# Optimization experiments

Measured on AMD Instinct MI355X. Metric: run time of the kernel, lower is better.

## Reference

```python
import math
import jax, jax.numpy as jnp
from jax import lax
import numpy as np

C = 256; A = 3; NIMG = 2; L = 5
SIZES = [(200, 304), (100, 152), (50, 76), (25, 38), (13, 19)]
STRIDES = [4, 8, 16, 32, 64]
LVTOP = 600          # cfg['lvtop'] (eval)
IMTOP = 300          # cfg['imtop1'] (eval)
SCORE_THR = 0.0      # cfg['score_thr1']
MIN_SIZE = 1e-2      # cfg['min_size1']
IOU_THR = 0.7        # cfg['iou_thr1']
IMH, IMW = 800.0, 1216.0
BBOX_CLIP = math.log(1000.0 / 16.0)   # clamp=True in decode_boxes
GROUP_OFF = 4096.0                     # > max canvas coord -> disjoint NMS groups


def _level_anchors(h, w, stride):
    scale = stride * 8.0
    r = np.array([0.5, 1.0, 2.0])
    ws = scale * np.sqrt(r); hs = scale / np.sqrt(r)          # [A]
    ys, xs = np.meshgrid(np.arange(h), np.arange(w), indexing='ij')
    cx = (xs.reshape(-1, 1) + 0.5) * stride                    # [HW,1]
    cy = (ys.reshape(-1, 1) + 0.5) * stride
    a = np.stack([cx - ws / 2, cy - hs / 2, cx + ws / 2, cy + hs / 2], axis=-1)
    return a.reshape(-1, 4).astype(np.float32)                 # [HW*A,4]


def setup_inputs() -> dict:
    key = jax.random.key(0)
    ks = jax.random.split(key, 10)
    inp = {}
    for i, (h, w) in enumerate(SIZES):
        inp[f'fmap{i}'] = jax.random.normal(ks[i], (NIMG, C, h, w), jnp.float32)
        inp[f'priors{i}'] = jnp.asarray(_level_anchors(h, w, STRIDES[i]))
    inp['imsizes'] = jnp.array([[IMH, IMW]] * NIMG, jnp.float32)   # (h, w) per image
    inp['conv_w'] = jax.random.normal(ks[5], (C, C, 3, 3), jnp.float32) * 0.03
    inp['conv_b'] = jnp.zeros((C,), jnp.float32)
    inp['log_w'] = jax.random.normal(ks[6], (A, C), jnp.float32) * 0.03
    inp['log_b'] = jnp.zeros((A,), jnp.float32)
    inp['reg_w'] = jax.random.normal(ks[7], (A * 4, C), jnp.float32) * 0.01
    inp['reg_b'] = jnp.zeros((A * 4,), jnp.float32)
    return inp


def _decode(reg, pri):
    pw = pri[..., 2] - pri[..., 0]; ph = pri[..., 3] - pri[..., 1]
    pcx = pri[..., 0] + 0.5 * pw;   pcy = pri[..., 1] + 0.5 * ph
    dx, dy = reg[..., 0], reg[..., 1]
    dw = jnp.minimum(reg[..., 2], BBOX_CLIP)
    dh = jnp.minimum(reg[..., 3], BBOX_CLIP)
    cx = dx * pw + pcx; cy = dy * ph + pcy
    w = pw * jnp.exp(dw); h = ph * jnp.exp(dh)
    return jnp.stack([cx - 0.5 * w, cy - 0.5 * h, cx + 0.5 * w, cy + 0.5 * h], axis=-1)


def _forward(fmaps, priors, imsizes, conv_w, conv_b, log_w, log_b, reg_w, reg_b):
    dn = ('NCHW', 'OIHW', 'NCHW')
    boxes_l, score_l = [], []
    for x, pri in zip(fmaps, priors):
        n = x.shape[0]
        h = jax.nn.relu(lax.conv_general_dilated(x, conv_w, (1, 1), 'SAME',
                                                 dimension_numbers=dn)
                        + conv_b[None, :, None, None])
        logit = (jnp.einsum('nchw,ac->nahw', h, log_w)
                 + log_b[None, :, None, None]).transpose(0, 2, 3, 1).reshape(n, -1)
        reg = (jnp.einsum('nchw,ac->nahw', h, reg_w)
               + reg_b[None, :, None, None]).transpose(0, 2, 3, 1).reshape(n, -1, 4)
        vals, top = lax.top_k(logit, LVTOP)                        # per-level topk
        reg_g = jnp.take_along_axis(reg, jnp.broadcast_to(top[:, :, None], (n, LVTOP, 4)), axis=1)
        pri_g = pri[top]                                           # [n,k,4]
        boxes_l.append(_decode(reg_g, pri_g))
        score_l.append(jax.nn.sigmoid(vals))
    boxes = jnp.concatenate(boxes_l, axis=1)                       # [n, L*k, 4]
    obj = jnp.concatenate(score_l, axis=1)                         # [n, L*k]
    n, dim = boxes.shape[0], boxes.shape[1]
    Nall = n * dim
    boxes = boxes.reshape(Nall, 4); obj = obj.reshape(Nall)
    imidx = jnp.arange(Nall) // dim
    lvl = jnp.tile(jnp.repeat(jnp.arange(L), LVTOP), n)
    valid = obj >= SCORE_THR
    sz = imsizes[imidx]                                            # [Nall,2] (h,w)
    boxes = jnp.stack([jnp.clip(boxes[:, 0], 0.0, sz[:, 1]),
                       jnp.clip(boxes[:, 1], 0.0, sz[:, 0]),
                       jnp.clip(boxes[:, 2], 0.0, sz[:, 1]),
                       jnp.clip(boxes[:, 3], 0.0, sz[:, 0])], axis=-1)
    valid = valid & (boxes[:, 2] - boxes[:, 0] >= MIN_SIZE) & (boxes[:, 3] - boxes[:, 1] >= MIN_SIZE)
    groups = imidx * 10 + lvl                                      # batched_nms groups
    # sort by score, invalid entries pushed to the end
    order = jnp.argsort(-jnp.where(valid, obj, -1.0))
    b = boxes[order]; v = valid[order]; g = groups[order]; im = imidx[order]
    # group-offset trick == torchvision batched_nms
    ob = b + g.astype(b.dtype)[:, None] * GROUP_OFF
    area = (ob[:, 2] - ob[:, 0]) * (ob[:, 3] - ob[:, 1])
    lt = jnp.maximum(ob[:, None, :2], ob[None, :, :2])
    rb = jnp.minimum(ob[:, None, 2:], ob[None, :, 2:])
    wh = jnp.maximum(rb - lt, 0.0)
    inter = wh[..., 0] * wh[..., 1]
    iou = lax.stop_gradient(inter / (area[:, None] + area[None, :] - inter))
    idxr = jnp.arange(Nall)
    def body(i, keep):
        sup = jnp.any(keep & (iou[i] > IOU_THR) & (idxr < i))
        return keep.at[i].set(v[i] & ~sup)
    keep = lax.fori_loop(0, Nall, body, jnp.zeros((Nall,), bool))
    # per-image cap at IMTOP (keep is already in score order)
    sel = keep[None, :] & (im[None, :] == jnp.arange(n)[:, None])  # [n,Nall]
    sel = sel & (jnp.cumsum(sel, axis=1) <= IMTOP)
    prio = jnp.where(sel, Nall - idxr[None, :], 0)
    pvals, pos = lax.top_k(prio, IMTOP)                            # [n,IMTOP]
    vout = pvals > 0
    bout = jnp.where(vout[..., None], b[pos], 0.0)                 # [n,IMTOP,4]
    imout = jnp.broadcast_to(jnp.arange(n)[:, None], (n, IMTOP)).reshape(-1).astype(jnp.int32)
    return bout.reshape(-1, 4), imout, vout.reshape(-1)


def reference(fmap0, fmap1, fmap2, fmap3, fmap4,
              priors0, priors1, priors2, priors3, priors4,
              imsizes, conv_w, conv_b, log_w, log_b, reg_w, reg_b):
    return _forward([fmap0, fmap1, fmap2, fmap3, fmap4],
                    [priors0, priors1, priors2, priors3, priors4],
                    imsizes, conv_w, conv_b, log_w, log_b, reg_w, reg_b)
```

## Files before the change

kernel.cpp:

```cpp
#include <hip/hip_runtime.h>
#include <math.h>

typedef unsigned long long u64;
typedef unsigned int u32;
typedef unsigned short u16;
typedef _Float16 f16;
typedef __attribute__((ext_vector_type(8))) _Float16 f16x8;
typedef __attribute__((ext_vector_type(8))) unsigned short ushort8;
typedef __attribute__((ext_vector_type(4))) float f32x4;

#define LVTOP 600
#define IMTOP 300
#define NIMG 2
#define NLVL 5
#define NCAND (NLVL*LVTOP)

__constant__ int d_HW[5]    = {60800,15200,3800,950,247};
__constant__ int d_LGOFF[5] = {0,364800,456000,478800,484500};
__constant__ int d_RGOFF[5] = {0,1459200,1824000,1915200,1938000};
__constant__ int d_H[5]  = {200,100,50,25,13};
__constant__ int d_W[5]  = {304,152,76,38,19};
__constant__ int d_TX[5] = {5,3,2,1,1};
__constant__ long d_XB[5] = {0, 31129600, 38912000, 40857600, 41344000};
__constant__ long d_CB[5] = {0, 3891200, 4864000, 5107200, 5168000};
__constant__ int d_SB[6] = {0,64,80,84,85,86};
#define NCHUNK 5183808
#define WS_NEED 178889200ull

__device__ __forceinline__ u32 okey(float f){
  u32 u = __float_as_uint(f);
  return (u & 0x80000000u) ? ~u : (u | 0x80000000u);
}

__device__ __forceinline__ void f16_split(float v, u16& hb, u16& lb){
  f16 h = (f16)v;
  float r = v - (float)h;
  f16 l = (f16)r;
  hb = __builtin_bit_cast(u16, h);
  lb = __builtin_bit_cast(u16, l);
}

__device__ __forceinline__ u64 shfl64(u64 v, int src){
  u32 lo = __shfl((u32)v, src);
  u32 hi = __shfl((u32)(v >> 32), src);
  return ((u64)hi << 32) | lo;
}

__device__ __forceinline__ void dma16(const u16* g, u16* l){
  __builtin_amdgcn_global_load_lds(
      (const __attribute__((address_space(1))) u32*)g,
      (__attribute__((address_space(3))) u32*)l, 16, 0, 0);
}

template<int NN, int NT>
__device__ void bitonic_desc64(u64* a, int tid){
  for (int k = 2; k <= NN; k <<= 1){
    for (int j = k >> 1; j > 0; j >>= 1){
      __syncthreads();
      for (int i = tid; i < NN; i += NT){
        int ixj = i ^ j;
        if (ixj > i){
          u64 x = a[i], y = a[ixj];
          bool up = ((i & k) == 0);
          if (up ? (x < y) : (x > y)){ a[i] = y; a[ixj] = x; }
        }
      }
    }
  }
  __syncthreads();
}

template<int NN, int NT>
__device__ void bitonic_asc32(u32* a, int tid){
  for (int k = 2; k <= NN; k <<= 1){
    for (int j = k >> 1; j > 0; j >>= 1){
      __syncthreads();
      for (int i = tid; i < NN; i += NT){
        int ixj = i ^ j;
        if (ixj > i){
          u32 x = a[i], y = a[ixj];
          bool up = ((i & k) == 0);
          if (up ? (x > y) : (x < y)){ a[i] = y; a[ixj] = x; }
        }
      }
    }
  }
  __syncthreads();
}

__device__ void suffix_scan(u32* s, int NB, int tid){
  for (int off = 1; off < NB; off <<= 1){
    u32 v0 = 0, v1 = 0;
    int i1 = tid + 1024;
    if (tid < NB) v0 = s[tid] + ((tid + off < NB) ? s[tid + off] : 0u);
    if (i1  < NB) v1 = s[i1]  + ((i1  + off < NB) ? s[i1  + off] : 0u);
    __syncthreads();
    if (tid < NB) s[tid] = v0;
    if (i1  < NB) s[i1]  = v1;
    __syncthreads();
  }
}

__global__ __launch_bounds__(256) void wprep(
    const float* __restrict__ cw, const float* __restrict__ lw,
    const float* __restrict__ rw, u16* __restrict__ wT, u16* __restrict__ whB,
    u32* __restrict__ ghist)
{
  int t = threadIdx.x;
  if (blockIdx.x < 72){
    int id = blockIdx.x*256 + t;
    int cc = id & 7;
    int co = (id >> 3) & 255;
    int tap = id >> 11;
    int ntg = co >> 4;
    size_t base = (size_t)((tap*8 + cc)*16 + ntg) * 1024;
    #pragma unroll
    for (int ci = 0; ci < 32; ci++){
      float v = cw[(size_t)co*2304 + (size_t)(cc*32 + ci)*9 + tap];
      u16 hi, lo; f16_split(v, hi, lo);
      int q = ci >> 3, j = ci & 7;
      int lane = q*16 + (co & 15);
      wT[base + lane*8 + j] = hi;
      wT[base + 512 + lane*8 + j] = lo;
    }
  } else if (blockIdx.x == 72){
    if (t < 128){
      int ks = t >> 4, nn = t & 15;
      for (int ci = 0; ci < 32; ci++){
        int k = ks*32 + ci;
        float v = 0.0f;
        if (nn < 3) v = lw[nn*256 + k];
        else if (nn < 15) v = rw[(nn-3)*256 + k];
        u16 hi, lo; f16_split(v, hi, lo);
        int q = ci >> 3, j = ci & 7;
        int lane = q*16 + nn;
        whB[ks*1024 + lane*8 + j] = hi;
        whB[ks*1024 + 512 + lane*8 + j] = lo;
      }
    }
  } else {
    int z = (blockIdx.x - 73)*1024 + t;
    #pragma unroll
    for (int q = 0; q < 4; q++){
      int i = z + q*256;
      if (i < NLVL*NIMG*2048) ghist[i] = 0;
    }
  }
}

__global__ __launch_bounds__(256) void xsplit(
    const float* __restrict__ f0, const float* __restrict__ f1,
    const float* __restrict__ f2, const float* __restrict__ f3,
    const float* __restrict__ f4,
    u16* __restrict__ xh, u16* __restrict__ xl, u16* __restrict__ zp)
{
  long id = (long)blockIdx.x*256 + threadIdx.x;
  if (blockIdx.x == 0 && threadIdx.x < 8) zp[threadIdx.x] = 0;
  if (id >= NCHUNK) return;
  int l = (id < d_CB[1]) ? 0 : (id < d_CB[2]) ? 1 : (id < d_CB[3]) ? 2 : (id < d_CB[4]) ? 3 : 4;
  long rem = id - d_CB[l];
  int HW = d_HW[l];
  int n = (int)(rem / (32*HW));
  int r2 = (int)(rem - (long)n*32*HW);
  int cg = r2 / HW;
  int p = r2 - cg*HW;
  const float* fm = (l==0)?f0:(l==1)?f1:(l==2)?f2:(l==3)?f3:f4;
  const float* gp = fm + ((size_t)(n*256 + cg*8))*HW + p;
  ushort8 hv, lv;
  #pragma unroll
  for (int j = 0; j < 8; j++){
    float v = gp[(size_t)j*HW];
    u16 hb, lb; f16_split(v, hb, lb);
    hv[j] = hb; lv[j] = lb;
  }
  *(ushort8*)&xh[id*8] = hv;
  *(ushort8*)&xl[id*8] = lv;
}

__global__ __launch_bounds__(256, 3) void conv_mfma(
    const float* __restrict__ f0, const float* __restrict__ f1,
    const float* __restrict__ f2, const float* __restrict__ f3,
    const float* __restrict__ f4,
    const u16* __restrict__ xh, const u16* __restrict__ xl,
    const u16* __restrict__ zp,
    const u16* __restrict__ wT, const u16* __restrict__ whB,
    const float* __restrict__ cb, const float* __restrict__ lb,
    const float* __restrict__ rb,
    float* __restrict__ lgb, float* __restrict__ rgb, int use_dma)
{
  __shared__ __align__(16) u16 smem[26624];

  const int t = threadIdx.x;
  const int n = blockIdx.y;
  int bx = blockIdx.x;
  int l, rbk;
  if (bx < 1000){ l = 0; rbk = bx; }
  else if (bx < 1300){ l = 1; rbk = bx - 1000; }
  else if (bx < 1400){ l = 2; rbk = bx - 1300; }
  else if (bx < 1425){ l = 3; rbk = bx - 1400; }
  else { l = 4; rbk = bx - 1425; }
  const int H = d_H[l], W = d_W[l], tilesX = d_TX[l];
  const int ty = rbk / tilesX;
  const int x0 = (rbk - ty*tilesX) * 64;
  const float* fm = (l==0) ? f0 : (l==1) ? f1 : (l==2) ? f2 : (l==3) ? f3 : f4;

  const int wave = t >> 6, lane = t & 63;
  const int quad = lane >> 4, l15 = lane & 15;
  const int HWp = H * W;
  const float* xin = fm + (size_t)n * 256 * HWp;

  f32x4 acc[4][4];
  #pragma unroll
  for (int a = 0; a < 4; a++)
    #pragma unroll
    for (int b = 0; b < 4; b++) acc[a][b] = (f32x4){0.f,0.f,0.f,0.f};

  auto compute_cc = [&](int cc, int bufo){
    #pragma unroll
    for (int ky = 0; ky < 3; ky++){
      #pragma unroll
      for (int kx = 0; kx < 3; kx++){
        int o0 = bufo + ((quad*3 + ky)*68 + (l15 + kx))*8;
        f16x8 Ah[4], Al[4];
        #pragma unroll
        for (int mt = 0; mt < 4; mt++){
          Ah[mt] = *(const f16x8*)&smem[o0 + mt*128];
          Al[mt] = *(const f16x8*)&smem[o0 + 6656 + mt*128];
        }
        const u16* bt = wT + (size_t)((((ky*3+kx)*8 + cc)*16) + wave*4) * 1024 + lane*8;
        #pragma unroll
        for (int nt = 0; nt < 4; nt++){
          f16x8 Bh = *(const f16x8*)(bt + nt*1024);
          f16x8 Bl = *(const f16x8*)(bt + nt*1024 + 512);
          #pragma unroll
          for (int mt = 0; mt < 4; mt++){
            acc[mt][nt] = __builtin_amdgcn_mfma_f32_16x16x32_f16(Ah[mt], Bh, acc[mt][nt], 0,0,0);
            acc[mt][nt] = __builtin_amdgcn_mfma_f32_16x16x32_f16(Al[mt], Bh, acc[mt][nt], 0,0,0);
            acc[mt][nt] = __builtin_amdgcn_mfma_f32_16x16x32_f16(Ah[mt], Bl, acc[mt][nt], 0,0,0);
          }
        }
      }
    }
  };

  if (use_dma){
    const u16* ph[4]; const u16* pl[4]; u32 pstep[4]; int dsth[4]; int kv[4];
    #pragma unroll
    for (int s = 0; s < 4; s++){
      int k = wave + s*4;
      kv[s] = (k < 13);
      int g = k*64 + lane;
      int gg = (g < 816) ? g : 0;
      int cg = gg / 204; int rem = gg - cg*204;
      int r = rem / 68;  int xi = rem - r*68;
      int gy = ty - 1 + r, gx = x0 - 1 + xi;
      bool inb = (g < 816) && (gy >= 0) && (gy < H) && (gx >= 0) && (gx < W);
      int gy2 = gy < 0 ? 0 : (gy >= H ? H-1 : gy);
      int gx2 = gx < 0 ? 0 : (gx >= W ? W-1 : gx);
      long off = d_XB[l] + (((long)(n*32 + cg))*HWp + (long)gy2*W + gx2)*8;
      ph[s] = inb ? (xh + off) : zp;
      pl[s] = inb ? (xl + off) : zp;
      pstep[s] = inb ? (u32)(32*HWp) : 0u;
      dsth[s] = k*512;
    }
    auto stage = [&](int bufo){
      #pragma unroll
      for (int s = 0; s < 4; s++){
        if (kv[s]){
          dma16(ph[s], &smem[bufo + dsth[s]]);
          dma16(pl[s], &smem[bufo + 6656 + dsth[s]]);
          ph[s] += pstep[s]; pl[s] += pstep[s];
        }
      }
    };
    stage(0);
    __syncthreads();
    for (int cc = 0; cc < 8; cc++){
      if (cc < 7) stage(((cc+1)&1)*13312);
      compute_cc(cc, (cc&1)*13312);
      __syncthreads();
    }
  } else {
    for (int cc = 0; cc < 8; cc++){
      __syncthreads();
      #pragma unroll
      for (int it = 0; it < 4; it++){
        int G = t + it*256;
        if (G < 816){
          int cg = G / 204; int rem = G - cg*204;
          int r = rem / 68; int xi = rem - r*68;
          int gy = ty - 1 + r, gx = x0 - 1 + xi;
          bool inb = (gy >= 0) & (gy < H) & (gx >= 0) & (gx < W);
          const float* gp = xin + (size_t)(cc*32 + cg*8) * HWp
                          + (size_t)(gy < 0 ? 0 : gy) * W + (gx < 0 ? 0 : gx);
          ushort8 hv, lv;
          #pragma unroll
          for (int j = 0; j < 8; j++){
            float v = inb ? gp[(size_t)j * HWp] : 0.0f;
            u16 hb, lb2; f16_split(v, hb, lb2);
            hv[j] = hb; lv[j] = lb2;
          }
          int off = ((cg*3 + r)*68 + xi)*8;
          *(ushort8*)&smem[off] = hv;
          *(ushort8*)&smem[6656 + off] = lv;
        }
      }
      __syncthreads();
      compute_cc(cc, 0);
    }
    __syncthreads();
  }

  u16* hA_h = smem;
  u16* hA_l = smem + 8704;
  f32x4 a2 = (f32x4){0.f,0.f,0.f,0.f};
  #pragma unroll
  for (int half = 0; half < 2; half++){
    if ((wave >> 1) == half){
      #pragma unroll
      for (int mt = 0; mt < 4; mt++){
        #pragma unroll
        for (int nt = 0; nt < 4; nt++){
          int col = (wave & 1)*64 + nt*16 + l15;
          float bias = cb[half*128 + col];
          #pragma unroll
          for (int r = 0; r < 4; r++){
            float h = fmaxf(acc[mt][nt][r] + bias, 0.0f);
            u16 hb, lb2; f16_split(h, hb, lb2);
            int pos = mt*16 + quad*4 + r;
            hA_h[pos*136 + col] = hb;
            hA_l[pos*136 + col] = lb2;
          }
        }
      }
    }
    __syncthreads();
    #pragma unroll
    for (int ks2 = 0; ks2 < 4; ks2++){
      int ks = half*4 + ks2;
      int ao = (wave*16 + l15)*136 + ks2*32 + quad*8;
      f16x8 Ah = *(const f16x8*)&hA_h[ao];
      f16x8 Al = *(const f16x8*)&hA_l[ao];
      const u16* wb = whB + ks*1024 + lane*8;
      f16x8 Bh = *(const f16x8*)wb;
      f16x8 Bl = *(const f16x8*)(wb + 512);
      a2 = __builtin_amdgcn_mfma_f32_16x16x32_f16(Ah, Bh, a2, 0,0,0);
      a2 = __builtin_amdgcn_mfma_f32_16x16x32_f16(Al, Bh, a2, 0,0,0);
      a2 = __builtin_amdgcn_mfma_f32_16x16x32_f16(Ah, Bl, a2, 0,0,0);
    }
    __syncthreads();
  }

  float* sm_out = (float*)smem;
  {
    int o = l15;
    float bias = (o < 3) ? lb[o] : ((o < 15) ? rb[o-3] : 0.0f);
    #pragma unroll
    for (int r = 0; r < 4; r++){
      int pos = wave*16 + quad*4 + r;
      sm_out[pos*16 + o] = a2[r] + bias;
    }
  }
  __syncthreads();
  {
    int P = W - x0; if (P > 64) P = 64;
    size_t pbase = (size_t)ty * W + x0;
    float* lg = lgb + d_LGOFF[l] + (size_t)n*HWp*3  + pbase*3;
    float* rg = rgb + d_RGOFF[l] + (size_t)n*HWp*12 + pbase*12;
    for (int j = t; j < P*3; j += 256)  lg[j] = sm_out[(j/3)*16 + (j%3)];
    for (int j = t; j < P*12; j += 256) rg[j] = sm_out[(j/12)*16 + 3 + (j%12)];
  }
}

__global__ __launch_bounds__(256) void hist1(
    const float* __restrict__ lg, u32* __restrict__ ghist)
{
  __shared__ u32 lh[2048];
  int t = threadIdx.x;
  int b = blockIdx.x, n = blockIdx.y;
  int l = (b < d_SB[1]) ? 0 : (b < d_SB[2]) ? 1 : (b < d_SB[3]) ? 2 : (b < d_SB[4]) ? 3 : 4;
  int s = b - d_SB[l], nsl = d_SB[l+1] - d_SB[l];
  int N = d_HW[l] * 3;
  const float* lgl = lg + d_LGOFF[l] + (size_t)n * N;
  for (int i = t; i < 2048; i += 256) lh[i] = 0;
  __syncthreads();
  int lo = (int)((long)N * s / nsl), hi = (int)((long)N * (s+1) / nsl);
  for (int i = lo + t; i < hi; i += 256)
    atomicAdd(&lh[okey(lgl[i]) >> 21], 1u);
  __syncthreads();
  u32* gh = ghist + (size_t)(l*NIMG + n) * 2048;
  for (int i = t; i < 2048; i += 256)
    if (lh[i]) atomicAdd(&gh[i], lh[i]);
}

__global__ __launch_bounds__(1024) void topk_decode(
    const float* __restrict__ lg, const float* __restrict__ rg,
    const float* __restrict__ pr0, const float* __restrict__ pr1,
    const float* __restrict__ pr2, const float* __restrict__ pr3,
    const float* __restrict__ pr4,
    const float* __restrict__ imsizes, const u32* __restrict__ ghist,
    float* __restrict__ cbox, float* __restrict__ cscore, u32* __restrict__ cvalid)
{
  __shared__ u32 hist[2048];
  __shared__ u32 sscan[2048];
  __shared__ u64 sel[1024];
  __shared__ u32 eqbuf[1024];
  __shared__ u32 scal[8];
  int tid = threadIdx.x;
  int l = blockIdx.x / NIMG;
  int n = blockIdx.x - l*NIMG;
  int HW = d_HW[l];
  int N = HW * 3;
  const float* lgl = lg + d_LGOFF[l] + (size_t)n * N;

  {
    const u32* gh = ghist + (size_t)blockIdx.x * 2048;
    for (int i = tid; i < 2048; i += 1024){ u32 h = gh[i]; hist[i] = h; sscan[i] = h; }
  }
  __syncthreads();
  suffix_scan(sscan, 2048, tid);
  if (tid < 2048){
    u32 Si = sscan[tid], Sn = (tid+1 < 2048) ? sscan[tid+1] : 0u;
    if (Si >= LVTOP && Sn < LVTOP){ scal[0] = (u32)tid; scal[1] = Si - hist[tid]; }
  }
  { int i2 = tid + 1024;
    u32 Si = sscan[i2], Sn = (i2+1 < 2048) ? sscan[i2+1] : 0u;
    if (Si >= LVTOP && Sn < LVTOP){ scal[0] = (u32)i2; scal[1] = Si - hist[i2]; } }
  __syncthreads();
  u32 B1 = scal[0], base1 = scal[1];

  for (int i = tid; i < 2048; i += 1024) hist[i] = 0;
  __syncthreads();
  for (int i = tid; i < N; i += 1024){
    u32 k = okey(lgl[i]);
    if ((k >> 21) == B1) atomicAdd(&hist[(k >> 10) & 0x7FFu], 1u);
  }
  __syncthreads();
  for (int i = tid; i < 2048; i += 1024) sscan[i] = hist[i];
  __syncthreads();
  suffix_scan(sscan, 2048, tid);
  {
    u32 need = LVTOP - base1;
    if (tid < 2048){
      u32 Si = sscan[tid], Sn = (tid+1 < 2048) ? sscan[tid+1] : 0u;
      if (Si >= need && Sn < need){ scal[2] = (u32)tid; scal[3] = base1 + Si - hist[tid]; }
    }
    int i2 = tid + 1024;
    u32 Si = sscan[i2], Sn = (i2+1 < 2048) ? sscan[i2+1] : 0u;
    if (Si >= need && Sn < need){ scal[2] = (u32)i2; scal[3] = base1 + Si - hist[i2]; }
  }
  __syncthreads();
  u32 B2 = scal[2], base2 = scal[3];

  for (int i = tid; i < 1024; i += 1024) hist[i] = 0;
  __syncthreads();
  u32 hi21 = (B1 << 11) | B2;
  for (int i = tid; i < N; i += 1024){
    u32 k = okey(lgl[i]);
    if ((k >> 10) == hi21) atomicAdd(&hist[k & 0x3FFu], 1u);
  }
  __syncthreads();
  for (int i = tid; i < 1024; i += 1024) sscan[i] = hist[i];
  __syncthreads();
  suffix_scan(sscan, 1024, tid);
  {
    u32 need = LVTOP - base2;
    if (tid < 1024){
      u32 Si = sscan[tid], Sn = (tid+1 < 1024) ? sscan[tid+1] : 0u;
      if (Si >= need && Sn < need){
        scal[4] = (hi21 << 10) | (u32)tid;
        scal[5] = base2 + Si - hist[tid];
      }
    }
  }
  if (tid == 0){ scal[6] = 0; scal[7] = 0; }
  __syncthreads();
  u32 T = scal[4], nAbove = scal[5], needEq = LVTOP - scal[5];

  for (int i = tid; i < 1024; i += 1024) sel[i] = 0;
  __syncthreads();
  for (int i = tid; i < N; i += 1024){
    u32 k = okey(lgl[i]);
    if (k > T){
      u32 p = atomicAdd(&scal[6], 1u);
      sel[p] = ((u64)k << 32) | (0xFFFFFFFFu - (u32)i);
    } else if (k == T){
      u32 p = atomicAdd(&scal[7], 1u);
      if (p < 1024) eqbuf[p] = (u32)i;
    }
  }
  __syncthreads();
  u32 cntE = scal[7];
  if (cntE > needEq){
    u32 m = cntE < 1024u ? cntE : 1024u;
    for (int i = tid; i < 1024; i += 1024) if ((u32)i >= m) eqbuf[i] = 0xFFFFFFFFu;
    __syncthreads();
    bitonic_asc32<1024,1024>(eqbuf, tid);
  }
  __syncthreads();
  if ((u32)tid < needEq)
    sel[nAbove + tid] = ((u64)T << 32) | (0xFFFFFFFFu - eqbuf[tid]);
  __syncthreads();
  bitonic_desc64<1024,1024>(sel, tid);

  if (tid < LVTOP){
    u64 c = sel[tid];
    u32 i = 0xFFFFFFFFu - (u32)c;
    float val = lgl[i];
    float score = 1.0f / (1.0f + expf(-val));
    int pp = (int)i / 3, a = (int)i - pp*3;
    const float* pri;
    if (l == 0) pri = pr0; else if (l == 1) pri = pr1; else if (l == 2) pri = pr2;
    else if (l == 3) pri = pr3; else pri = pr4;
    pri += (size_t)i * 4;
    const float* rgp = rg + d_RGOFF[l] + ((size_t)n * HW + pp) * 12 + a * 4;
    float px0 = pri[0], py0 = pri[1], px1 = pri[2], py1 = pri[3];
    float pw = px1 - px0, ph = py1 - py0;
    float pcx = px0 + 0.5f*pw, pcy = py0 + 0.5f*ph;
    const float BC = (float)4.135166556742356;
    float dx = rgp[0], dy = rgp[1];
    float dw = fminf(rgp[2], BC), dh = fminf(rgp[3], BC);
    float cx = dx*pw + pcx, cy = dy*ph + pcy;
    float bw = pw * expf(dw), bh = ph * expf(dh);
    float x1 = cx - 0.5f*bw, y1 = cy - 0.5f*bh;
    float x2 = cx + 0.5f*bw, y2 = cy + 0.5f*bh;
    float imh = imsizes[n*2+0], imw = imsizes[n*2+1];
    x1 = fminf(fmaxf(x1, 0.0f), imw);
    y1 = fminf(fmaxf(y1, 0.0f), imh);
    x2 = fminf(fmaxf(x2, 0.0f), imw);
    y2 = fminf(fmaxf(y2, 0.0f), imh);
    u32 valid = (score >= 0.0f) && ((x2 - x1) >= 1e-2f) && ((y2 - y1) >= 1e-2f);
    int ci = n*NCAND + l*LVTOP + tid;
    cbox[ci*4+0] = x1; cbox[ci*4+1] = y1; cbox[ci*4+2] = x2; cbox[ci*4+3] = y2;
    cscore[ci] = score; cvalid[ci] = valid;
  }
}

__global__ __launch_bounds__(1024) void sort_cand(
    const float* __restrict__ cscore, const u32* __restrict__ cvalid,
    const float* __restrict__ cbox,
    float* __restrict__ sbox, float* __restrict__ sob,
    float* __restrict__ sarea, u32* __restrict__ svalid,
    u32* __restrict__ rlist, u32* __restrict__ kflag)
{
  __shared__ u64 a[4096];
  int tid = threadIdx.x, n = blockIdx.x;
  for (int i = tid; i < 4096; i += 1024){
    if (i < NCAND){
      int ci = n*NCAND + i;
      float s = cvalid[ci] ? cscore[ci] : -1.0f;
      a[i] = ((u64)okey(s) << 32) | (0xFFFFFFFFu - (u32)i);
    } else a[i] = 0;
  }
  bitonic_desc64<4096,1024>(a, tid);
  int mylvl[3];
  #pragma unroll
  for (int q = 0; q < 3; q++){
    int r = tid + q*1024;
    mylvl[q] = 0;
    if (r < NCAND){
      u32 li = 0xFFFFFFFFu - (u32)a[r];
      int ci = n*NCAND + (int)li;
      float b0 = cbox[ci*4+0], b1 = cbox[ci*4+1], b2 = cbox[ci*4+2], b3 = cbox[ci*4+3];
      int lvl = (int)li / LVTOP;
      mylvl[q] = lvl;
      float off = (float)(n*10 + lvl) * 4096.0f;
      int so = n*NCAND + r;
      sbox[so*4+0]=b0; sbox[so*4+1]=b1; sbox[so*4+2]=b2; sbox[so*4+3]=b3;
      float o0=b0+off, o1=b1+off, o2=b2+off, o3=b3+off;
      sob[so*4+0]=o0; sob[so*4+1]=o1; sob[so*4+2]=o2; sob[so*4+3]=o3;
      sarea[so] = (o2-o0)*(o3-o1);
      svalid[so] = cvalid[ci];
    }
  }
  __syncthreads();
  #pragma unroll
  for (int q = 0; q < 3; q++){
    int r = tid + q*1024;
    a[r] = (r < NCAND) ? (1ull << (12*mylvl[q])) : 0ull;
  }
  a[tid + 3072] = 0ull;
  __syncthreads();
  for (int off = 1; off < 4096; off <<= 1){
    u64 v[4];
    #pragma unroll
    for (int q = 0; q < 4; q++){
      int i = tid + q*1024;
      v[q] = a[i] + ((i >= off) ? a[i-off] : 0ull);
    }
    __syncthreads();
    #pragma unroll
    for (int q = 0; q < 4; q++) a[tid + q*1024] = v[q];
    __syncthreads();
  }
  #pragma unroll
  for (int q = 0; q < 3; q++){
    int r = tid + q*1024;
    if (r < NCAND){
      int lv = mylvl[q];
      int pos = (int)((a[r] >> (12*lv)) & 0xFFFull) - 1;
      rlist[(n*NLVL + lv)*LVTOP + pos] = (u32)r;
      kflag[n*NCAND + r] = 0u;
    }
  }
}

__global__ __launch_bounds__(256) void nms_mask_l(
    const float* __restrict__ sob, const float* __restrict__ sarea,
    const u32* __restrict__ svalid, const u32* __restrict__ rlist,
    u64* __restrict__ pmask)
{
  __shared__ float sj[64*5];
  int tid = threadIdx.x;
  int nl = blockIdx.y;
  int n = nl / NLVL;
  int i = blockIdx.x*256 + tid;
  bool act = false;
  float oi0=0, oi1=0, oi2=0, oi3=0, ai=0;
  if (i < LVTOP){
    int so = n*NCAND + (int)rlist[nl*LVTOP + i];
    act = svalid[so] != 0;
    oi0 = sob[so*4+0]; oi1 = sob[so*4+1]; oi2 = sob[so*4+2]; oi3 = sob[so*4+3];
    ai = sarea[so];
  }
  for (int w = 0; w < 10; w++){
    __syncthreads();
    if (tid < 64){
      int j = w*64 + tid;
      if (j < LVTOP){
        int so = n*NCAND + (int)rlist[nl*LVTOP + j];
        sj[tid*5+0]=sob[so*4+0]; sj[tid*5+1]=sob[so*4+1];
        sj[tid*5+2]=sob[so*4+2]; sj[tid*5+3]=sob[so*4+3];
        sj[tid*5+4]=sarea[so];
      }
    }
    __syncthreads();
    if (act){
      u64 bits = 0;
      int jj0 = (i >= w*64) ? (i - w*64 + 1) : 0;
      int jjend = (LVTOP - w*64 < 64) ? (LVTOP - w*64) : 64;
      for (int jj = jj0; jj < jjend; jj++){
        float oj0=sj[jj*5+0], oj1=sj[jj*5+1], oj2=sj[jj*5+2], oj3=sj[jj*5+3], aj=sj[jj*5+4];
        float ltx = fmaxf(oi0, oj0), lty = fmaxf(oi1, oj1);
        float rbx = fminf(oi2, oj2), rby = fminf(oi3, oj3);
        float wx = fmaxf(rbx - ltx, 0.0f), wy = fmaxf(rby - lty, 0.0f);
        float inter = wx * wy;
        float iou = inter / ((ai + aj) - inter);
        if (iou > 0.7f) bits |= (1ull << jj);
      }
      pmask[((size_t)(nl*LVTOP + i))*10 + w] = bits;
    }
  }
}

__global__ __launch_bounds__(64) void nms_scan_l(
    const u64* __restrict__ pmask, const u32* __restrict__ svalid,
    const u32* __restrict__ rlist, u32* __restrict__ kflag)
{
  int t = threadIdx.x, nl = blockIdx.x, n = nl / NLVL;
  u64 vw = 0, remv = 0;
  for (int c = 0; c < 10; c++){
    int i = c*64 + t;
    int pred = 0;
    if (i < LVTOP) pred = svalid[n*NCAND + (int)rlist[nl*LVTOP + i]] != 0;
    u64 b = __ballot(pred);
    if (t == c) vw = b;
  }
  for (int w = 0; w < 10; w++){
    u64 act = shfl64(vw, w) & ~shfl64(remv, w);
    while (act){
      int bpos = __builtin_ctzll(act);
      int i = w*64 + bpos;
      if (t == 0) kflag[n*NCAND + (int)rlist[nl*LVTOP + i]] = 1u;
      u64 m = (t < 10) ? pmask[((size_t)(nl*LVTOP + i))*10 + t] : 0ull;
      remv |= m;
      act &= ~(1ull << bpos);
      act &= ~shfl64(m, w);
    }
  }
}

__global__ __launch_bounds__(1024) void merge_out(
    const u32* __restrict__ kflag, const float* __restrict__ sbox,
    float* __restrict__ out)
{
  __shared__ u32 ps[4096];
  int tid = threadIdx.x, n = blockIdx.x;
  u32 f[4];
  #pragma unroll
  for (int q = 0; q < 4; q++){
    int i = tid + q*1024;
    f[q] = (i < NCAND) ? kflag[n*NCAND + i] : 0u;
    ps[i] = f[q];
  }
  __syncthreads();
  for (int off = 1; off < 4096; off <<= 1){
    u32 v[4];
    #pragma unroll
    for (int q = 0; q < 4; q++){
      int i = tid + q*1024;
      v[q] = ps[i] + ((i >= off) ? ps[i-off] : 0u);
    }
    __syncthreads();
    #pragma unroll
    for (int q = 0; q < 4; q++) ps[tid + q*1024] = v[q];
    __syncthreads();
  }
  #pragma unroll
  for (int q = 0; q < 4; q++){
    int i = tid + q*1024;
    if (i < NCAND && f[q] && ps[i] <= IMTOP){
      int slot = n*IMTOP + (int)ps[i] - 1;
      int so = n*NCAND + i;
      out[slot*4+0] = sbox[so*4+0]; out[slot*4+1] = sbox[so*4+1];
      out[slot*4+2] = sbox[so*4+2]; out[slot*4+3] = sbox[so*4+3];
    }
  }
  u32 kept = ps[NCAND-1]; if (kept > IMTOP) kept = IMTOP;
  for (int j = tid; j < IMTOP; j += 1024){
    int slot = n*IMTOP + j;
    if ((u32)j >= kept){
      out[slot*4+0]=0; out[slot*4+1]=0; out[slot*4+2]=0; out[slot*4+3]=0;
    }
    out[2400 + slot] = (float)n;
    out[3000 + slot] = ((u32)j < kept) ? 1.0f : 0.0f;
  }
}

extern "C" void kernel_launch(void* const* d_in, const int* in_sizes, int n_in,
                              void* d_out, int out_size, void* d_ws, size_t ws_size,
                              hipStream_t stream)
{
  const float* fmap[5]   = {(const float*)d_in[0], (const float*)d_in[2], (const float*)d_in[4],
                            (const float*)d_in[6], (const float*)d_in[8]};
  const float* priors[5] = {(const float*)d_in[1], (const float*)d_in[3], (const float*)d_in[5],
                            (const float*)d_in[7], (const float*)d_in[9]};
  const float* imsz   = (const float*)d_in[10];
  const float* conv_w = (const float*)d_in[11];
  const float* conv_b = (const float*)d_in[12];
  const float* log_w  = (const float*)d_in[13];
  const float* log_b  = (const float*)d_in[14];
  const float* reg_w  = (const float*)d_in[15];
  const float* reg_b  = (const float*)d_in[16];

  char* base = (char*)d_ws;
  float* lg     = (float*)(base + 0);
  float* rg     = (float*)(base + 1943928);
  float* cscore = (float*)(base + 9719640);
  float* cbox   = (float*)(base + 9743640);
  u32*   cvalid = (u32*)  (base + 9839640);
  float* sbox   = (float*)(base + 9863640);
  float* sob    = (float*)(base + 9959640);
  float* sarea  = (float*)(base + 10055640);
  u32*   svalid = (u32*)  (base + 10079640);
  u32*   rlist  = (u32*)  (base + 10103640);
  u32*   kflag  = (u32*)  (base + 10127640);
  u64*   pmask  = (u64*)  (base + 10151648);
  u32*   ghist  = (u32*)  (base + 10151648);
  u16*   wT     = (u16*)  (base + 10631648);
  u16*   whB    = (u16*)  (base + 12990944);
  u16*   zp     = (u16*)  (base + 13007328);
  u16*   xh     = (u16*)  (base + 13007344);
  u16*   xl     = (u16*)  (base + 95948272);

  int use_dma = (ws_size >= WS_NEED) ? 1 : 0;

  wprep<<<93, 256, 0, stream>>>(conv_w, log_w, reg_w, wT, whB, ghist);
  if (use_dma)
    xsplit<<<(NCHUNK + 255)/256, 256, 0, stream>>>(
        fmap[0], fmap[1], fmap[2], fmap[3], fmap[4], xh, xl, zp);

  conv_mfma<<<dim3(1438, NIMG), 256, 0, stream>>>(
      fmap[0], fmap[1], fmap[2], fmap[3], fmap[4],
      xh, xl, zp, wT, whB, conv_b, log_b, reg_b, lg, rg, use_dma);

  hist1<<<dim3(86, NIMG), 256, 0, stream>>>(lg, ghist);

  topk_decode<<<NLVL*NIMG, 1024, 0, stream>>>(lg, rg,
      priors[0], priors[1], priors[2], priors[3], priors[4],
      imsz, ghist, cbox, cscore, cvalid);
  sort_cand<<<NIMG, 1024, 0, stream>>>(cscore, cvalid, cbox, sbox, sob, sarea,
                                       svalid, rlist, kflag);
  nms_mask_l<<<dim3(3, NIMG*NLVL), 256, 0, stream>>>(sob, sarea, svalid, rlist, pmask);
  nms_scan_l<<<NIMG*NLVL, 64, 0, stream>>>(pmask, svalid, rlist, kflag);
  merge_out<<<NIMG, 1024, 0, stream>>>(kflag, sbox, (float*)d_out);
}
```

Baseline: 1.325 ms.

## Prefetch conv weight fragments one step ahead and stage NMS masks in LDS

The conv MFMA inner loop now loads the next B-fragment (weights) from global memory while issuing MFMAs on the current one, hiding global load latency behind compute. The per-level NMS scan kernel first copies its whole suppression mask block into shared memory with 256 threads, then runs the serial scan from LDS instead of doing dependent global loads and shuffles on each iteration. The prefetch costs extra registers, which could lower occupancy or cause spills. The scan kernel gains a bulk copy and uses about 48KB of LDS per block.

```diff
diff --git a/kernel.cpp b/kernel.cpp
--- a/kernel.cpp
+++ b/kernel.cpp
@@ -216,28 +216,32 @@
     for (int b = 0; b < 4; b++) acc[a][b] = (f32x4){0.f,0.f,0.f,0.f};
 
   auto compute_cc = [&](int cc, int bufo){
-    #pragma unroll
-    for (int ky = 0; ky < 3; ky++){
+    const u16* btb = wT + (size_t)((cc*16) + wave*4) * 1024 + lane*8;
+    f16x8 Bh = *(const f16x8*)(btb);
+    f16x8 Bl = *(const f16x8*)(btb + 512);
+    #pragma unroll
+    for (int tap = 0; tap < 9; tap++){
+      const int ky = tap / 3, kx = tap - ky*3;
+      int o0 = bufo + ((quad*3 + ky)*68 + (l15 + kx))*8;
+      f16x8 Ah[4], Al[4];
       #pragma unroll
-      for (int kx = 0; kx < 3; kx++){
-        int o0 = bufo + ((quad*3 + ky)*68 + (l15 + kx))*8;
-        f16x8 Ah[4], Al[4];
+      for (int mt = 0; mt < 4; mt++){
+        Ah[mt] = *(const f16x8*)&smem[o0 + mt*128];
+        Al[mt] = *(const f16x8*)&smem[o0 + 6656 + mt*128];
+      }
+      const u16* bt = btb + (size_t)tap * (8*16*1024);
+      #pragma unroll
+      for (int nt = 0; nt < 4; nt++){
+        f16x8 cBh = Bh, cBl = Bl;
+        const u16* np = (nt < 3) ? (bt + (nt+1)*1024)
+                      : ((tap < 8) ? (bt + 8*16*1024) : bt);
+        Bh = *(const f16x8*)np;
+        Bl = *(const f16x8*)(np + 512);
         #pragma unroll
         for (int mt = 0; mt < 4; mt++){
-          Ah[mt] = *(const f16x8*)&smem[o0 + mt*128];
-          Al[mt] = *(const f16x8*)&smem[o0 + 6656 + mt*128];
-        }
-        const u16* bt = wT + (size_t)((((ky*3+kx)*8 + cc)*16) + wave*4) * 1024 + lane*8;
-        #pragma unroll
-        for (int nt = 0; nt < 4; nt++){
-          f16x8 Bh = *(const f16x8*)(bt + nt*1024);
-          f16x8 Bl = *(const f16x8*)(bt + nt*1024 + 512);
-          #pragma unroll
-          for (int mt = 0; mt < 4; mt++){
-            acc[mt][nt] = __builtin_amdgcn_mfma_f32_16x16x32_f16(Ah[mt], Bh, acc[mt][nt], 0,0,0);
-            acc[mt][nt] = __builtin_amdgcn_mfma_f32_16x16x32_f16(Al[mt], Bh, acc[mt][nt], 0,0,0);
-            acc[mt][nt] = __builtin_amdgcn_mfma_f32_16x16x32_f16(Ah[mt], Bl, acc[mt][nt], 0,0,0);
-          }
+          acc[mt][nt] = __builtin_amdgcn_mfma_f32_16x16x32_f16(Ah[mt], cBh, acc[mt][nt], 0,0,0);
+          acc[mt][nt] = __builtin_amdgcn_mfma_f32_16x16x32_f16(Al[mt], cBh, acc[mt][nt], 0,0,0);
+          acc[mt][nt] = __builtin_amdgcn_mfma_f32_16x16x32_f16(Ah[mt], cBl, acc[mt][nt], 0,0,0);
         }
       }
     }
@@ -653,29 +657,36 @@
   }
 }
 
-__global__ __launch_bounds__(64) void nms_scan_l(
+__global__ __launch_bounds__(256) void nms_scan_l(
     const u64* __restrict__ pmask, const u32* __restrict__ svalid,
     const u32* __restrict__ rlist, u32* __restrict__ kflag)
 {
+  __shared__ u64 pm[LVTOP*10];
   int t = threadIdx.x, nl = blockIdx.x, n = nl / NLVL;
-  u64 vw = 0, remv = 0;
-  for (int c = 0; c < 10; c++){
-    int i = c*64 + t;
-    int pred = 0;
-    if (i < LVTOP) pred = svalid[n*NCAND + (int)rlist[nl*LVTOP + i]] != 0;
-    u64 b = __ballot(pred);
-    if (t == c) vw = b;
-  }
-  for (int w = 0; w < 10; w++){
-    u64 act = shfl64(vw, w) & ~shfl64(remv, w);
-    while (act){
-      int bpos = __builtin_ctzll(act);
-      int i = w*64 + bpos;
-      if (t == 0) kflag[n*NCAND + (int)rlist[nl*LVTOP + i]] = 1u;
-      u64 m = (t < 10) ? pmask[((size_t)(nl*LVTOP + i))*10 + t] : 0ull;
-      remv |= m;
-      act &= ~(1ull << bpos);
-      act &= ~shfl64(m, w);
+  const u64* gpm = pmask + (size_t)nl * LVTOP * 10;
+  for (int i = t; i < LVTOP*10; i += 256) pm[i] = gpm[i];
+  __syncthreads();
+  if (t < 64){
+    u64 vw = 0, remv = 0;
+    for (int c = 0; c < 10; c++){
+      int i = c*64 + t;
+      int pred = 0;
+      if (i < LVTOP) pred = svalid[n*NCAND + (int)rlist[nl*LVTOP + i]] != 0;
+      u64 b = __ballot(pred);
+      if (t == c) vw = b;
+    }
+    for (int w = 0; w < 10; w++){
+      u64 act = shfl64(vw, w) & ~shfl64(remv, w);
+      while (act){
+        int bpos = __builtin_ctzll(act);
+        int i = w*64 + bpos;
+        if (t == 0) kflag[n*NCAND + (int)rlist[nl*LVTOP + i]] = 1u;
+        u64 m = (t < 10) ? pm[i*10 + t] : 0ull;
+        u64 mw = pm[i*10 + w];
+        remv |= m;
+        act &= ~(1ull << bpos);
+        act &= ~mw;
+      }
     }
   }
 }
@@ -782,6 +793,6 @@
   sort_cand<<<NIMG, 1024, 0, stream>>>(cscore, cvalid, cbox, sbox, sob, sarea,
                                        svalid, rlist, kflag);
   nms_mask_l<<<dim3(3, NIMG*NLVL), 256, 0, stream>>>(sob, sarea, svalid, rlist, pmask);
-  nms_scan_l<<<NIMG*NLVL, 64, 0, stream>>>(pmask, svalid, rlist, kflag);
+  nms_scan_l<<<NIMG*NLVL, 256, 0, stream>>>(pmask, svalid, rlist, kflag);
   merge_out<<<NIMG, 1024, 0, stream>>>(kflag, sbox, (float*)d_out);
 }
```

Result: faster. 1.212 ms (-8.5%).
